# Performance work log

Measured on AMD Instinct MI355X. Metric: run time of the kernel, lower is better.

The kernel has to match this reference:

```python
import jax, jax.numpy as jnp
import numpy as np

I, H, O = 32, 64, 8  # input_size, hidden_layer, output_size
B, T = 4096, 256


def setup_inputs() -> dict:
    key = jax.random.key(0)
    ks = jax.random.split(key, 7)
    s_ih = 1.0 / np.sqrt(H)
    return {
        "x": jax.random.normal(ks[0], (B, T, I), dtype=jnp.float32),
        # PyTorch nn.LSTM params, gate order [i, f, g, o]
        "W_ih": jax.random.uniform(ks[1], (4 * H, I), jnp.float32, -s_ih, s_ih),
        "W_hh": jax.random.uniform(ks[2], (4 * H, H), jnp.float32, -s_ih, s_ih),
        "b_ih": jax.random.uniform(ks[3], (4 * H,), jnp.float32, -s_ih, s_ih),
        "b_hh": jax.random.uniform(ks[4], (4 * H,), jnp.float32, -s_ih, s_ih),
        "W_fc": jax.random.uniform(ks[5], (O, H), jnp.float32, -s_ih, s_ih),
        "b_fc": jax.random.uniform(ks[6], (O,), jnp.float32, -s_ih, s_ih),
    }


def reference(x, W_ih, W_hh, b_ih, b_hh, W_fc, b_fc):
    # Precompute input-to-hidden projections for all timesteps in one GEMM.
    # [B, T, 4H]
    x_proj = jnp.einsum('bti,gi->btg', x, W_ih) + b_ih + b_hh

    def step(carry, xp_t):
        h, c = carry  # [B, H] each
        gates = xp_t + h @ W_hh.T  # [B, 4H]
        i_g, f_g, g_g, o_g = jnp.split(gates, 4, axis=-1)
        i_g = jax.nn.sigmoid(i_g)
        f_g = jax.nn.sigmoid(f_g)
        g_g = jnp.tanh(g_g)
        o_g = jax.nn.sigmoid(o_g)
        c = f_g * c + i_g * g_g
        h = o_g * jnp.tanh(c)
        return (h, c), None

    h0 = jnp.zeros((x.shape[0], H), dtype=x.dtype)
    c0 = jnp.zeros((x.shape[0], H), dtype=x.dtype)
    # scan over time axis: move T to leading axis
    (h_T, c_T), _ = jax.lax.scan(step, (h0, c0), jnp.swapaxes(x_proj, 0, 1))
    # out[:, -1, :] == final hidden state for single-layer batch_first LSTM
    return h_T @ W_fc.T + b_fc
```

## Files before the change

### kernel.cpp

```cpp
#include <hip/hip_runtime.h>
#include <hip/hip_bf16.h>


#define T_LEN 256
#define I_SZ  32
#define H_SZ  64
#define O_SZ  8
#define BR    16
#define HS    72

typedef __attribute__((ext_vector_type(8))) short short8;
typedef __attribute__((ext_vector_type(4))) float f32x4;

static __device__ __forceinline__ unsigned fbits(float f) {
    union { float f; unsigned u; } v; v.f = f; return v.u;
}
static __device__ __forceinline__ unsigned pk2t(float lo, float hi) {
    return __builtin_amdgcn_perm(fbits(hi), fbits(lo), 0x07060302u);
}
static __device__ __forceinline__ short f2bf_rne(float f) {
    union { __hip_bfloat16 b; short s; } u;
    u.b = __float2bfloat16(f);
    return u.s;
}
static __device__ __forceinline__ f32x4 rcp4(f32x4 d) {
    f32x4 r;
    r.x = __builtin_amdgcn_rcpf(d.x);
    r.y = __builtin_amdgcn_rcpf(d.y);
    r.z = __builtin_amdgcn_rcpf(d.z);
    r.w = __builtin_amdgcn_rcpf(d.w);
    return r;
}
static __device__ __forceinline__ f32x4 exp2_4(f32x4 m) {
    f32x4 e;
    e.x = __builtin_amdgcn_exp2f(m.x);
    e.y = __builtin_amdgcn_exp2f(m.y);
    e.z = __builtin_amdgcn_exp2f(m.z);
    e.w = __builtin_amdgcn_exp2f(m.w);
    return e;
}
static __device__ __forceinline__ f32x4 clamp4(f32x4 x, float lo, float hi) {
    f32x4 r;
    r.x = __builtin_amdgcn_fmed3f(x.x, lo, hi);
    r.y = __builtin_amdgcn_fmed3f(x.y, lo, hi);
    r.z = __builtin_amdgcn_fmed3f(x.z, lo, hi);
    r.w = __builtin_amdgcn_fmed3f(x.w, lo, hi);
    return r;
}
#define LOG2E     1.4426950408889634f
#define TWO_LOG2E 2.8853900817779268f

static __device__ __forceinline__ f32x4 sig4(f32x4 x) {
    f32x4 e = exp2_4(x * (-LOG2E));
    return rcp4(e + 1.0f);
}
static __device__ __forceinline__ f32x4 tanh4(f32x4 x) {
    f32x4 xc = clamp4(x, -10.0f, 10.0f);
    f32x4 e  = exp2_4(xc * TWO_LOG2E);
    return (e - 1.0f) * rcp4(e + 1.0f);
}

__global__ __launch_bounds__(256, 1)
void lstm_fused_kernel(const float* __restrict__ x,
                       const float* __restrict__ W_ih,
                       const float* __restrict__ W_hh,
                       const float* __restrict__ b_ih,
                       const float* __restrict__ b_hh,
                       const float* __restrict__ W_fc,
                       const float* __restrict__ b_fc,
                       float* __restrict__ out)
{
    __shared__ short hbuf[2][BR][HS];
    __shared__ float Hf[BR][64];

    const int tid   = threadIdx.x;
    const int wave  = tid >> 6;
    const int lane  = tid & 63;
    const int quad  = lane >> 4;
    const int nlow  = lane & 15;
    const int jw    = wave * 16 + nlow;
    const int rbase = quad * 4;
    const int b0    = blockIdx.x * BR;

    short8 bfrag[4][3];
    f32x4  biasf[4];
    for (int g = 0; g < 4; ++g) {
        const int col = g * 64 + jw;
        {
            const float* wr = W_ih + col * I_SZ + quad * 8;
            short8 f;
            #pragma unroll
            for (int e = 0; e < 8; ++e) f[e] = f2bf_rne(wr[e]);
            bfrag[g][0] = f;
        }
        #pragma unroll
        for (int kt = 1; kt < 3; ++kt) {
            const float* wr = W_hh + col * H_SZ + (kt - 1) * 32 + quad * 8;
            short8 f;
            #pragma unroll
            for (int e = 0; e < 8; ++e) f[e] = f2bf_rne(wr[e]);
            bfrag[g][kt] = f;
        }
        const float bg = b_ih[col] + b_hh[col];
        biasf[g] = (f32x4){bg, bg, bg, bg};
    }

    for (int q = tid; q < 2 * BR * HS; q += 256) ((short*)hbuf)[q] = (short)0;

    const float* xb = x + ((size_t)(b0 + nlow) * T_LEN) * I_SZ + quad * 8;

    float4 nx[16];
    short8 sc[8];
    #pragma unroll
    for (int s = 0; s < 8; ++s) {
        nx[2*s]   = *(const float4*)(xb + s * I_SZ);
        nx[2*s+1] = *(const float4*)(xb + s * I_SZ + 4);
    }
    #pragma unroll
    for (int s = 0; s < 8; ++s) {
        union { uint4 u; short8 v; } w;
        w.u.x = pk2t(nx[2*s].x,   nx[2*s].y);
        w.u.y = pk2t(nx[2*s].z,   nx[2*s].w);
        w.u.z = pk2t(nx[2*s+1].x, nx[2*s+1].y);
        w.u.w = pk2t(nx[2*s+1].z, nx[2*s+1].w);
        sc[s] = w.v;
    }

    const short* rb[2] = { &hbuf[0][nlow][quad * 8], &hbuf[1][nlow][quad * 8] };
    short*       wb[2] = { &hbuf[0][rbase][jw],      &hbuf[1][rbase][jw] };

    f32x4 cc = {0.f, 0.f, 0.f, 0.f};
    f32x4 hh = {0.f, 0.f, 0.f, 0.f};

    for (int ch = 0; ch < 32; ++ch) {
        #pragma unroll
        for (int tc = 0; tc < 8; ++tc) {
            const int t = ch * 8 + tc;

            __syncthreads();

            const short* hr = rb[t & 1];
            short8 a1 = *(const short8*)(hr);
            short8 a2 = *(const short8*)(hr + 32);

            if (tc == 0 && ch + 1 < 32) {
                const float* nxt = xb + (t + 8) * I_SZ;
                #pragma unroll
                for (int s = 0; s < 8; ++s) {
                    nx[2*s]   = *(const float4*)(nxt + s * I_SZ);
                    nx[2*s+1] = *(const float4*)(nxt + s * I_SZ + 4);
                }
            }

            const short8 ax = sc[tc];

            f32x4 acc[4];
            #pragma unroll
            for (int g = 0; g < 4; ++g) {
                f32x4 a = __builtin_amdgcn_mfma_f32_16x16x32_bf16(ax, bfrag[g][0], biasf[g], 0, 0, 0);
                a = __builtin_amdgcn_mfma_f32_16x16x32_bf16(a1, bfrag[g][1], a, 0, 0, 0);
                a = __builtin_amdgcn_mfma_f32_16x16x32_bf16(a2, bfrag[g][2], a, 0, 0, 0);
                acc[g] = a;
            }

            if (tc == 7 && ch + 1 < 32) {
                #pragma unroll
                for (int s = 0; s < 8; ++s) {
                    union { uint4 u; short8 v; } w;
                    w.u.x = pk2t(nx[2*s].x,   nx[2*s].y);
                    w.u.y = pk2t(nx[2*s].z,   nx[2*s].w);
                    w.u.z = pk2t(nx[2*s+1].x, nx[2*s+1].y);
                    w.u.w = pk2t(nx[2*s+1].z, nx[2*s+1].w);
                    sc[s] = w.v;
                }
            }

            f32x4 iv = sig4(acc[0]);
            f32x4 fv = sig4(acc[1]);
            f32x4 gv = tanh4(acc[2]);
            f32x4 ov = sig4(acc[3]);
            cc = __builtin_elementwise_fma(fv, cc, iv * gv);
            hh = ov * tanh4(cc);

            short* hw = wb[(t + 1) & 1];
            hw[0 * HS] = (short)((fbits(hh.x) + 0x8000u) >> 16);
            hw[1 * HS] = (short)((fbits(hh.y) + 0x8000u) >> 16);
            hw[2 * HS] = (short)((fbits(hh.z) + 0x8000u) >> 16);
            hw[3 * HS] = (short)((fbits(hh.w) + 0x8000u) >> 16);
        }
    }

    Hf[rbase + 0][jw] = hh.x;
    Hf[rbase + 1][jw] = hh.y;
    Hf[rbase + 2][jw] = hh.z;
    Hf[rbase + 3][jw] = hh.w;
    __syncthreads();

    if (tid < BR * O_SZ) {
        const int r = tid >> 3;
        const int o = tid & 7;
        const float* wf = W_fc + o * H_SZ;
        float acc = b_fc[o];
        #pragma unroll
        for (int jx = 0; jx < H_SZ; ++jx) acc += Hf[r][jx] * wf[jx];
        out[(size_t)(b0 + r) * O_SZ + o] = acc;
    }
}

extern "C" void kernel_launch(void* const* d_in, const int* in_sizes, int n_in,
                              void* d_out, int out_size, void* d_ws, size_t ws_size,
                              hipStream_t stream) {
    const float* x    = (const float*)d_in[0];
    const float* W_ih = (const float*)d_in[1];
    const float* W_hh = (const float*)d_in[2];
    const float* b_ih = (const float*)d_in[3];
    const float* b_hh = (const float*)d_in[4];
    const float* W_fc = (const float*)d_in[5];
    const float* b_fc = (const float*)d_in[6];
    float* out = (float*)d_out;

    const int B = 4096;
    lstm_fused_kernel<<<dim3(B / BR), dim3(256), 0, stream>>>(
        x, W_ih, W_hh, b_ih, b_hh, W_fc, b_fc, out);
}
```

Baseline: 288.0 us.

## Fold exp scaling into weights, merge reciprocals, and hoist input MFMA off critical path

Pre-scales the gate weights and biases by -log2(e) (or -2log2(e) for the g gate) so the exponent can be taken directly from the MFMA outputs. Merges the sigmoid*tanh products into a single reciprocal each, cutting rcp instructions per step. Computes the next timestep's input projection MFMA before the current step's activations, taking it off the recurrent dependency chain. In exchange, bf16 rounding now applies to the scaled weights, which shifts numerics slightly, and the tanh clamp range changes.

```diff
diff --git a/kernel.cpp b/kernel.cpp
--- a/kernel.cpp
+++ b/kernel.cpp
@@ -47,18 +47,13 @@
     r.w = __builtin_amdgcn_fmed3f(x.w, lo, hi);
     return r;
 }
+static __device__ __forceinline__ f32x4 fma4(f32x4 a, f32x4 b, f32x4 c) {
+    return __builtin_elementwise_fma(a, b, c);
+}
+
 #define LOG2E     1.4426950408889634f
 #define TWO_LOG2E 2.8853900817779268f
-
-static __device__ __forceinline__ f32x4 sig4(f32x4 x) {
-    f32x4 e = exp2_4(x * (-LOG2E));
-    return rcp4(e + 1.0f);
-}
-static __device__ __forceinline__ f32x4 tanh4(f32x4 x) {
-    f32x4 xc = clamp4(x, -10.0f, 10.0f);
-    f32x4 e  = exp2_4(xc * TWO_LOG2E);
-    return (e - 1.0f) * rcp4(e + 1.0f);
-}
+#define ECLAMP    28.8f
 
 __global__ __launch_bounds__(256, 1)
 void lstm_fused_kernel(const float* __restrict__ x,
@@ -85,12 +80,13 @@
     short8 bfrag[4][3];
     f32x4  biasf[4];
     for (int g = 0; g < 4; ++g) {
+        const float scale = (g == 2) ? -TWO_LOG2E : -LOG2E;
         const int col = g * 64 + jw;
         {
             const float* wr = W_ih + col * I_SZ + quad * 8;
             short8 f;
             #pragma unroll
-            for (int e = 0; e < 8; ++e) f[e] = f2bf_rne(wr[e]);
+            for (int e = 0; e < 8; ++e) f[e] = f2bf_rne(scale * wr[e]);
             bfrag[g][0] = f;
         }
         #pragma unroll
@@ -98,10 +94,10 @@
             const float* wr = W_hh + col * H_SZ + (kt - 1) * 32 + quad * 8;
             short8 f;
             #pragma unroll
-            for (int e = 0; e < 8; ++e) f[e] = f2bf_rne(wr[e]);
+            for (int e = 0; e < 8; ++e) f[e] = f2bf_rne(scale * wr[e]);
             bfrag[g][kt] = f;
         }
-        const float bg = b_ih[col] + b_hh[col];
+        const float bg = scale * (b_ih[col] + b_hh[col]);
         biasf[g] = (f32x4){bg, bg, bg, bg};
     }
 
@@ -132,6 +128,11 @@
     f32x4 cc = {0.f, 0.f, 0.f, 0.f};
     f32x4 hh = {0.f, 0.f, 0.f, 0.f};
 
+    f32x4 preacc[4];
+    #pragma unroll
+    for (int g = 0; g < 4; ++g)
+        preacc[g] = __builtin_amdgcn_mfma_f32_16x16x32_bf16(sc[0], bfrag[g][0], biasf[g], 0, 0, 0);
+
     for (int ch = 0; ch < 32; ++ch) {
         #pragma unroll
         for (int tc = 0; tc < 8; ++tc) {
@@ -152,13 +153,10 @@
                 }
             }
 
-            const short8 ax = sc[tc];
-
             f32x4 acc[4];
             #pragma unroll
             for (int g = 0; g < 4; ++g) {
-                f32x4 a = __builtin_amdgcn_mfma_f32_16x16x32_bf16(ax, bfrag[g][0], biasf[g], 0, 0, 0);
-                a = __builtin_amdgcn_mfma_f32_16x16x32_bf16(a1, bfrag[g][1], a, 0, 0, 0);
+                f32x4 a = __builtin_amdgcn_mfma_f32_16x16x32_bf16(a1, bfrag[g][1], preacc[g], 0, 0, 0);
                 a = __builtin_amdgcn_mfma_f32_16x16x32_bf16(a2, bfrag[g][2], a, 0, 0, 0);
                 acc[g] = a;
             }
@@ -175,12 +173,20 @@
                 }
             }
 
-            f32x4 iv = sig4(acc[0]);
-            f32x4 fv = sig4(acc[1]);
-            f32x4 gv = tanh4(acc[2]);
-            f32x4 ov = sig4(acc[3]);
-            cc = __builtin_elementwise_fma(fv, cc, iv * gv);
-            hh = ov * tanh4(cc);
+            const short8 nax = sc[(tc + 1) & 7];
+            #pragma unroll
+            for (int g = 0; g < 4; ++g)
+                preacc[g] = __builtin_amdgcn_mfma_f32_16x16x32_bf16(nax, bfrag[g][0], biasf[g], 0, 0, 0);
+
+            f32x4 ei = exp2_4(acc[0]);
+            f32x4 ef = exp2_4(acc[1]);
+            f32x4 eg = exp2_4(clamp4(acc[2], -ECLAMP, ECLAMP));
+            f32x4 eo = exp2_4(acc[3]);
+            f32x4 fv = rcp4(ef + 1.0f);
+            f32x4 ig = (1.0f - eg) * rcp4((ei + 1.0f) * (eg + 1.0f));
+            cc = fma4(fv, cc, ig);
+            f32x4 ec = exp2_4(clamp4(cc * (-TWO_LOG2E), -ECLAMP, ECLAMP));
+            hh = (1.0f - ec) * rcp4((eo + 1.0f) * (ec + 1.0f));
 
             short* hw = wb[(t + 1) & 1];
             hw[0 * HS] = (short)((fbits(hh.x) + 0x8000u) >> 16);
```

After: 282.1 us (median of 2 runs). 2.1% less time.
